# Performance work log

Hardware: AMD Instinct MI355X
Metric: run time of the kernel (lower is better)

## Reference

```python
import jax, jax.numpy as jnp
import numpy as np

B, S, D, H = 4, 2048, 1024, 16
DH = D // H  # 64


def setup_inputs() -> dict:
    key = jax.random.key(0)
    ks = jax.random.split(key, 7)
    scale = 1.0 / np.sqrt(DH)
    return {
        "sequences": jax.random.normal(ks[0], (B, S, D), dtype=jnp.float32),
        # torch Linear weights: [out, in] per head -> stacked [H, DH, DH]
        "Wq": jax.random.uniform(ks[1], (H, DH, DH), jnp.float32, -scale, scale),
        "bq": jax.random.uniform(ks[2], (H, DH), jnp.float32, -scale, scale),
        "Wk": jax.random.uniform(ks[3], (H, DH, DH), jnp.float32, -scale, scale),
        "bk": jax.random.uniform(ks[4], (H, DH), jnp.float32, -scale, scale),
        "Wv": jax.random.uniform(ks[5], (H, DH, DH), jnp.float32, -scale, scale),
        "bv": jax.random.uniform(ks[6], (H, DH), jnp.float32, -scale, scale),
    }


def reference(sequences, Wq, bq, Wk, bk, Wv, bv):
    # split d into heads: [B, S, H, DH]
    x = sequences.reshape(B, S, H, DH)
    # per-head Linear: y = x @ W.T + b
    q = jnp.einsum("bshd,hed->bshe", x, Wq) + bq
    k = jnp.einsum("bshd,hed->bshe", x, Wk) + bk
    v = jnp.einsum("bshd,hed->bshe", x, Wv) + bv
    # scaled dot-product attention per head
    scores = jnp.einsum("bshd,bthd->bhst", q, k) / jnp.sqrt(jnp.float32(DH))
    attn = jax.nn.softmax(scores, axis=-1)
    out = jnp.einsum("bhst,bthd->bshd", attn, v)
    # hstack heads back to [B, S, D]
    return out.reshape(B, S, D)
```

## Files before the change

kernel.cpp:

```cpp
#include <hip/hip_runtime.h>
#include <hip/hip_bf16.h>


typedef unsigned short u16;
typedef unsigned int   u32;
typedef float  f32x4  __attribute__((ext_vector_type(4)));
typedef __bf16 bf16x4 __attribute__((ext_vector_type(4)));
typedef __bf16 bf16x8 __attribute__((ext_vector_type(8)));

#define NB 4
#define SS 2048
#define DDIM 1024
#define NH 16
#define DH 64

static __device__ __forceinline__ float fexp2(float x) {
#if __has_builtin(__builtin_amdgcn_exp2f)
    return __builtin_amdgcn_exp2f(x);
#else
    return exp2f(x);
#endif
}
static __device__ __forceinline__ bf16x4 cvt4(f32x4 v) {
    return __builtin_convertvector(v, bf16x4);
}
static __device__ __forceinline__ bf16x8 cvt8(f32x4 lo, f32x4 hi) {
    return __builtin_shufflevector(cvt4(lo), cvt4(hi), 0, 1, 2, 3, 4, 5, 6, 7);
}

#define WST 72

__global__ __launch_bounds__(256) void qkv_kernel(
        const float* __restrict__ x,
        const float* __restrict__ Wq, const float* __restrict__ bq,
        const float* __restrict__ Wk, const float* __restrict__ bk,
        const float* __restrict__ Wv, const float* __restrict__ bv,
        u16* __restrict__ Qw, u16* __restrict__ Kw, u16* __restrict__ Vt) {
    __shared__ __align__(16) u16 W_lds[3 * DH * WST];

    const int tid  = threadIdx.x;
    const int w    = tid >> 6;
    const int lane = tid & 63;
    const int quad = lane >> 4;
    const int c    = lane & 15;
    const int bid  = blockIdx.x;
    const int bh   = bid & 63;
    const int s0   = (bid >> 6) * 256;
    const int b    = bh >> 4, h = bh & 15;

    {
        const float* Wsrc[3] = {Wq + h*DH*DH, Wk + h*DH*DH, Wv + h*DH*DH};
        #pragma unroll
        for (int j = 0; j < 6; ++j) {
            const int m = j >> 1;
            const int chunk = ((j & 1) << 8) + tid;
            const float* src = Wsrc[m] + chunk * 8;
            f32x4 lo = *(const f32x4*)src;
            f32x4 hi = *(const f32x4*)(src + 4);
            const int row = chunk >> 3, c8 = chunk & 7;
            *(bf16x8*)&W_lds[(m*DH + row) * WST + c8*8] = cvt8(lo, hi);
        }
    }
    __syncthreads();

    bf16x8 wf[3][4][2];
    #pragma unroll
    for (int m = 0; m < 3; ++m)
        #pragma unroll
        for (int mt = 0; mt < 4; ++mt)
            #pragma unroll
            for (int kh = 0; kh < 2; ++kh)
                wf[m][mt][kh] = *(const bf16x8*)&W_lds[(m*DH + mt*16 + c) * WST + kh*32 + quad*8];

    f32x4 biasQK[2][4];
    float biasV[4];
    #pragma unroll
    for (int mt = 0; mt < 4; ++mt) {
        biasQK[0][mt] = *(const f32x4*)(bq + h*DH + mt*16 + quad*4);
        biasQK[1][mt] = *(const f32x4*)(bk + h*DH + mt*16 + quad*4);
        biasV[mt] = bv[h*DH + mt*16 + c];
    }

    const size_t qkbase = (size_t)bh * SS * DH;
    const size_t vtbase = (size_t)bh * DH * SS;

    #pragma unroll 1
    for (int g = 0; g < 4; ++g) {
        const int sb = s0 + w*64 + g*16;
        const float* xr = x + ((size_t)(b * SS + sb + c)) * DDIM + h * DH;
        bf16x8 xb[2];
        #pragma unroll
        for (int kh = 0; kh < 2; ++kh) {
            f32x4 lo = *(const f32x4*)(xr + kh*32 + quad*8);
            f32x4 hi = *(const f32x4*)(xr + kh*32 + quad*8 + 4);
            xb[kh] = cvt8(lo, hi);
        }

        const int srow = sb + c;
        const int tq = srow & 31;
        const int sK = (srow & ~31) | ((tq & 4) << 2) | ((tq >> 3) << 2) | (tq & 3);

        #pragma unroll
        for (int m = 0; m < 2; ++m) {
            const float scale = (m == 0) ? 0.18033688f : 1.0f;
            u16* base = (m == 0 ? Qw : Kw) + qkbase + (size_t)(m == 0 ? srow : sK) * DH;
            #pragma unroll
            for (int mt = 0; mt < 4; ++mt) {
                f32x4 acc = {0.f, 0.f, 0.f, 0.f};
                acc = __builtin_amdgcn_mfma_f32_16x16x32_bf16(wf[m][mt][0], xb[0], acc, 0, 0, 0);
                acc = __builtin_amdgcn_mfma_f32_16x16x32_bf16(wf[m][mt][1], xb[1], acc, 0, 0, 0);
                f32x4 v = (acc + biasQK[m][mt]) * scale;
                *(bf16x4*)(base + mt*16 + quad*4) = cvt4(v);
            }
        }
        #pragma unroll
        for (int nt = 0; nt < 4; ++nt) {
            f32x4 acc = {0.f, 0.f, 0.f, 0.f};
            acc = __builtin_amdgcn_mfma_f32_16x16x32_bf16(xb[0], wf[2][nt][0], acc, 0, 0, 0);
            acc = __builtin_amdgcn_mfma_f32_16x16x32_bf16(xb[1], wf[2][nt][1], acc, 0, 0, 0);
            f32x4 v = acc + biasV[nt];
            u16* dst = Vt + vtbase + (size_t)(nt*16 + c) * SS + sb + quad*4;
            *(bf16x4*)dst = cvt4(v);
        }
    }
}

#define KT 128
#define KST 72
#define VST 136

#define LOAD_FRAGS(kf, vf, g) do {                                             \
        kf[0] = *(const bf16x8*)&Kl[((g)*32 + c) * KST + quad*8];              \
        kf[1] = *(const bf16x8*)&Kl[((g)*32 + c) * KST + 32 + quad*8];         \
        kf[2] = *(const bf16x8*)&Kl[((g)*32 + 16 + c) * KST + quad*8];         \
        kf[3] = *(const bf16x8*)&Kl[((g)*32 + 16 + c) * KST + 32 + quad*8];    \
        vf[0] = *(const bf16x8*)&Vl[( 0 + c) * VST + (g)*32 + quad*8];         \
        vf[1] = *(const bf16x8*)&Vl[(16 + c) * VST + (g)*32 + quad*8];         \
        vf[2] = *(const bf16x8*)&Vl[(32 + c) * VST + (g)*32 + quad*8];         \
        vf[3] = *(const bf16x8*)&Vl[(48 + c) * VST + (g)*32 + quad*8];         \
    } while (0)

#define COMPUTE_G(kf, vf) do {                                                 \
        __builtin_amdgcn_s_setprio(1);                                         \
        _Pragma("unroll")                                                      \
        for (int qt = 0; qt < 4; ++qt) {                                       \
            f32x4 sA = {0.f,0.f,0.f,0.f}, sB = {0.f,0.f,0.f,0.f};              \
            sA = __builtin_amdgcn_mfma_f32_16x16x32_bf16(kf[0], qf[qt][0], sA, 0,0,0); \
            sA = __builtin_amdgcn_mfma_f32_16x16x32_bf16(kf[1], qf[qt][1], sA, 0,0,0); \
            sB = __builtin_amdgcn_mfma_f32_16x16x32_bf16(kf[2], qf[qt][0], sB, 0,0,0); \
            sB = __builtin_amdgcn_mfma_f32_16x16x32_bf16(kf[3], qf[qt][1], sB, 0,0,0); \
            f32x4 eA, eB;                                                      \
            _Pragma("unroll")                                                  \
            for (int r = 0; r < 4; ++r) { eA[r] = fexp2(sA[r]); eB[r] = fexp2(sB[r]); } \
            bf16x8 pf = cvt8(eA, eB);                                          \
            o[0][qt] = __builtin_amdgcn_mfma_f32_16x16x32_bf16(vf[0], pf, o[0][qt], 0,0,0); \
            o[1][qt] = __builtin_amdgcn_mfma_f32_16x16x32_bf16(vf[1], pf, o[1][qt], 0,0,0); \
            o[2][qt] = __builtin_amdgcn_mfma_f32_16x16x32_bf16(vf[2], pf, o[2][qt], 0,0,0); \
            o[3][qt] = __builtin_amdgcn_mfma_f32_16x16x32_bf16(vf[3], pf, o[3][qt], 0,0,0); \
            lacc[qt] = __builtin_amdgcn_mfma_f32_16x16x32_bf16(ones8, pf, lacc[qt], 0,0,0); \
        }                                                                      \
        __builtin_amdgcn_s_setprio(0);                                         \
    } while (0)

__global__ __launch_bounds__(256, 2) void attn_kernel(
        const u16* __restrict__ Qw, const u16* __restrict__ Kw,
        const u16* __restrict__ Vt, float* __restrict__ out) {
    __shared__ __align__(16) u16 K_lds[2][KT * KST];
    __shared__ __align__(16) u16 V_lds[2][DH * VST];

    const int tid  = threadIdx.x;
    const int w    = tid >> 6;
    const int lane = tid & 63;
    const int quad = lane >> 4;
    const int c    = lane & 15;
    const int bid  = blockIdx.x;
    const int bh   = bid & 63;
    const int q0   = (bid >> 6) * 256;
    const int qw   = q0 + w * 64;

    const u16* Qb = Qw + (size_t)bh * SS * DH;
    const u16* Kb = Kw + (size_t)bh * SS * DH;
    const u16* Vb = Vt + (size_t)bh * DH * SS;

    bf16x8 qf[4][2];
    #pragma unroll
    for (int qt = 0; qt < 4; ++qt) {
        const u16* qrow = Qb + (size_t)(qw + qt*16 + c) * DH;
        qf[qt][0] = *(const bf16x8*)(qrow + quad*8);
        qf[qt][1] = *(const bf16x8*)(qrow + 32 + quad*8);
    }

    f32x4 o[4][4];
    f32x4 lacc[4];
    #pragma unroll
    for (int qt = 0; qt < 4; ++qt) {
        lacc[qt] = (f32x4){0.f, 0.f, 0.f, 0.f};
        #pragma unroll
        for (int dt = 0; dt < 4; ++dt) o[dt][qt] = (f32x4){0.f, 0.f, 0.f, 0.f};
    }

    bf16x8 ones8;
    { union { u16 u[8]; bf16x8 v; } one;
      #pragma unroll
      for (int i = 0; i < 8; ++i) one.u[i] = 0x3F80;
      ones8 = one.v; }

    const int krow = tid >> 1;
    const int kcol = (tid & 1) * 32;
    const int kofs = krow * KST + kcol;
    const int vrow = tid >> 2;
    const int vcol = (tid & 3) * 32;
    const int vofs = vrow * VST + vcol;

    uint4 kr0 = *(const uint4*)(Kb + (size_t)krow * DH + kcol);
    uint4 kr1 = *(const uint4*)(Kb + (size_t)krow * DH + kcol + 8);
    uint4 kr2 = *(const uint4*)(Kb + (size_t)krow * DH + kcol + 16);
    uint4 kr3 = *(const uint4*)(Kb + (size_t)krow * DH + kcol + 24);
    uint4 vr0 = *(const uint4*)(Vb + (size_t)vrow * SS + vcol);
    uint4 vr1 = *(const uint4*)(Vb + (size_t)vrow * SS + vcol + 8);
    uint4 vr2 = *(const uint4*)(Vb + (size_t)vrow * SS + vcol + 16);
    uint4 vr3 = *(const uint4*)(Vb + (size_t)vrow * SS + vcol + 24);

    #pragma unroll 1
    for (int t0 = 0; t0 < SS; t0 += KT) {
        const int bsel = (t0 >> 7) & 1;
        u16* Kl = K_lds[bsel];
        u16* Vl = V_lds[bsel];
        *(uint4*)&Kl[kofs]      = kr0;
        *(uint4*)&Kl[kofs + 8]  = kr1;
        *(uint4*)&Kl[kofs + 16] = kr2;
        *(uint4*)&Kl[kofs + 24] = kr3;
        *(uint4*)&Vl[vofs]      = vr0;
        *(uint4*)&Vl[vofs + 8]  = vr1;
        *(uint4*)&Vl[vofs + 16] = vr2;
        *(uint4*)&Vl[vofs + 24] = vr3;
        __syncthreads();
        int tn = t0 + KT; if (tn >= SS) tn = 0;
        kr0 = *(const uint4*)(Kb + (size_t)(tn + krow) * DH + kcol);
        kr1 = *(const uint4*)(Kb + (size_t)(tn + krow) * DH + kcol + 8);
        kr2 = *(const uint4*)(Kb + (size_t)(tn + krow) * DH + kcol + 16);
        kr3 = *(const uint4*)(Kb + (size_t)(tn + krow) * DH + kcol + 24);
        vr0 = *(const uint4*)(Vb + (size_t)vrow * SS + tn + vcol);
        vr1 = *(const uint4*)(Vb + (size_t)vrow * SS + tn + vcol + 8);
        vr2 = *(const uint4*)(Vb + (size_t)vrow * SS + tn + vcol + 16);
        vr3 = *(const uint4*)(Vb + (size_t)vrow * SS + tn + vcol + 24);

        bf16x8 kfA[4], vfA[4], kfB[4], vfB[4];
        LOAD_FRAGS(kfA, vfA, 0);
        LOAD_FRAGS(kfB, vfB, 1);
        COMPUTE_G(kfA, vfA);
        LOAD_FRAGS(kfA, vfA, 2);
        COMPUTE_G(kfB, vfB);
        LOAD_FRAGS(kfB, vfB, 3);
        COMPUTE_G(kfA, vfA);
        COMPUTE_G(kfB, vfB);
    }

    const int b = bh >> 4, h = bh & 15;
    #pragma unroll
    for (int qt = 0; qt < 4; ++qt) {
        const float inv = 1.0f / lacc[qt][0];
        const int token = qw + qt*16 + c;
        float* orow = out + ((size_t)b * SS + token) * DDIM + h * DH;
        #pragma unroll
        for (int dt = 0; dt < 4; ++dt) {
            f32x4 vv = o[dt][qt] * inv;
            *(f32x4*)(orow + dt*16 + quad*4) = vv;
        }
    }
}

extern "C" void kernel_launch(void* const* d_in, const int* in_sizes, int n_in,
                              void* d_out, int out_size, void* d_ws, size_t ws_size,
                              hipStream_t stream) {
    const float* x  = (const float*)d_in[0];
    const float* Wq = (const float*)d_in[1];
    const float* bq = (const float*)d_in[2];
    const float* Wk = (const float*)d_in[3];
    const float* bk = (const float*)d_in[4];
    const float* Wv = (const float*)d_in[5];
    const float* bv = (const float*)d_in[6];

    u16* Qw = (u16*)d_ws;
    u16* Kw = Qw + (size_t)NB * NH * SS * DH;
    u16* Vt = Kw + (size_t)NB * NH * SS * DH;

    qkv_kernel<<<64 * (SS / 256), 256, 0, stream>>>(
        x, Wq, bq, Wk, bk, Wv, bv, Qw, Kw, Vt);
    attn_kernel<<<64 * (SS / 256), 256, 0, stream>>>(Qw, Kw, Vt, (float*)d_out);
}
```

Measured before the change: 179.1 us.

## Switch attention inner loop to 32x32x16 MFMA tiles with VALU row sums

Replaces the 16x16x32 bf16 MFMA tiling in the attention kernel with 32x32x16 MFMAs for both QK^T and PV. The K-row permutation written by the projection kernel is changed so the score accumulator layout matches the PV operand layout. The softmax denominator is now summed with VALU adds plus a cross-half shuffle instead of an extra MFMA against a ones vector. The aim is fewer MFMA instructions and less fragment traffic per tile. The trade-off is larger 16-wide accumulators, which raise register pressure and may affect the two-blocks-per-CU occupancy target.

```diff
diff --git a/kernel.cpp b/kernel.cpp
--- a/kernel.cpp
+++ b/kernel.cpp
@@ -4,9 +4,10 @@
 
 typedef unsigned short u16;
 typedef unsigned int   u32;
-typedef float  f32x4  __attribute__((ext_vector_type(4)));
-typedef __bf16 bf16x4 __attribute__((ext_vector_type(4)));
-typedef __bf16 bf16x8 __attribute__((ext_vector_type(8)));
+typedef float  f32x4   __attribute__((ext_vector_type(4)));
+typedef float  f32x16  __attribute__((ext_vector_type(16)));
+typedef __bf16 bf16x4  __attribute__((ext_vector_type(4)));
+typedef __bf16 bf16x8  __attribute__((ext_vector_type(8)));
 
 #define NB 4
 #define SS 2048
@@ -98,7 +99,10 @@
 
         const int srow = sb + c;
         const int tq = srow & 31;
-        const int sK = (srow & ~31) | ((tq & 4) << 2) | ((tq >> 3) << 2) | (tq & 3);
+        const int sK = (srow & ~31) | (tq & 3)
+                     | (((tq >> 3) & 1) << 2)
+                     | (((tq >> 2) & 1) << 3)
+                     | (((tq >> 4) & 1) << 4);
 
         #pragma unroll
         for (int m = 0; m < 2; ++m) {
@@ -129,36 +133,41 @@
 #define KST 72
 #define VST 136
 
-#define LOAD_FRAGS(kf, vf, g) do {                                             \
-        kf[0] = *(const bf16x8*)&Kl[((g)*32 + c) * KST + quad*8];              \
-        kf[1] = *(const bf16x8*)&Kl[((g)*32 + c) * KST + 32 + quad*8];         \
-        kf[2] = *(const bf16x8*)&Kl[((g)*32 + 16 + c) * KST + quad*8];         \
-        kf[3] = *(const bf16x8*)&Kl[((g)*32 + 16 + c) * KST + 32 + quad*8];    \
-        vf[0] = *(const bf16x8*)&Vl[( 0 + c) * VST + (g)*32 + quad*8];         \
-        vf[1] = *(const bf16x8*)&Vl[(16 + c) * VST + (g)*32 + quad*8];         \
-        vf[2] = *(const bf16x8*)&Vl[(32 + c) * VST + (g)*32 + quad*8];         \
-        vf[3] = *(const bf16x8*)&Vl[(48 + c) * VST + (g)*32 + quad*8];         \
+#define Z16 {0.f,0.f,0.f,0.f,0.f,0.f,0.f,0.f,0.f,0.f,0.f,0.f,0.f,0.f,0.f,0.f}
+
+#define QT_BODY(qt, lp) do {                                                   \
+        f32x16 s = Z16;                                                        \
+        s = __builtin_amdgcn_mfma_f32_32x32x16_bf16(ka0, qf[qt][0], s, 0,0,0); \
+        s = __builtin_amdgcn_mfma_f32_32x32x16_bf16(ka1, qf[qt][1], s, 0,0,0); \
+        s = __builtin_amdgcn_mfma_f32_32x32x16_bf16(ka2, qf[qt][2], s, 0,0,0); \
+        s = __builtin_amdgcn_mfma_f32_32x32x16_bf16(ka3, qf[qt][3], s, 0,0,0); \
+        f32x16 e;                                                              \
+        _Pragma("unroll")                                                      \
+        for (int r = 0; r < 16; ++r) e[r] = fexp2(s[r]);                       \
+        lp += (((e[0]+e[1])+(e[2]+e[3])) + ((e[4]+e[5])+(e[6]+e[7])))          \
+            + (((e[8]+e[9])+(e[10]+e[11])) + ((e[12]+e[13])+(e[14]+e[15])));   \
+        bf16x8 pf0 = cvt8((f32x4){e[0],e[1],e[2],e[3]},                        \
+                          (f32x4){e[4],e[5],e[6],e[7]});                       \
+        bf16x8 pf1 = cvt8((f32x4){e[8],e[9],e[10],e[11]},                      \
+                          (f32x4){e[12],e[13],e[14],e[15]});                   \
+        o[0][qt] = __builtin_amdgcn_mfma_f32_32x32x16_bf16(vf00, pf0, o[0][qt], 0,0,0); \
+        o[0][qt] = __builtin_amdgcn_mfma_f32_32x32x16_bf16(vf01, pf1, o[0][qt], 0,0,0); \
+        o[1][qt] = __builtin_amdgcn_mfma_f32_32x32x16_bf16(vf10, pf0, o[1][qt], 0,0,0); \
+        o[1][qt] = __builtin_amdgcn_mfma_f32_32x32x16_bf16(vf11, pf1, o[1][qt], 0,0,0); \
     } while (0)
 
-#define COMPUTE_G(kf, vf) do {                                                 \
+#define GROUP(g) do {                                                          \
+        bf16x8 ka0 = *(const bf16x8*)&Kl[((g)*32 + l31) * KST +  0 + hi*8];    \
+        bf16x8 ka1 = *(const bf16x8*)&Kl[((g)*32 + l31) * KST + 16 + hi*8];    \
+        bf16x8 ka2 = *(const bf16x8*)&Kl[((g)*32 + l31) * KST + 32 + hi*8];    \
+        bf16x8 ka3 = *(const bf16x8*)&Kl[((g)*32 + l31) * KST + 48 + hi*8];    \
+        bf16x8 vf00 = *(const bf16x8*)&Vl[( 0 + l31) * VST + (g)*32 +  0 + hi*8]; \
+        bf16x8 vf01 = *(const bf16x8*)&Vl[( 0 + l31) * VST + (g)*32 + 16 + hi*8]; \
+        bf16x8 vf10 = *(const bf16x8*)&Vl[(32 + l31) * VST + (g)*32 +  0 + hi*8]; \
+        bf16x8 vf11 = *(const bf16x8*)&Vl[(32 + l31) * VST + (g)*32 + 16 + hi*8]; \
         __builtin_amdgcn_s_setprio(1);                                         \
-        _Pragma("unroll")                                                      \
-        for (int qt = 0; qt < 4; ++qt) {                                       \
-            f32x4 sA = {0.f,0.f,0.f,0.f}, sB = {0.f,0.f,0.f,0.f};              \
-            sA = __builtin_amdgcn_mfma_f32_16x16x32_bf16(kf[0], qf[qt][0], sA, 0,0,0); \
-            sA = __builtin_amdgcn_mfma_f32_16x16x32_bf16(kf[1], qf[qt][1], sA, 0,0,0); \
-            sB = __builtin_amdgcn_mfma_f32_16x16x32_bf16(kf[2], qf[qt][0], sB, 0,0,0); \
-            sB = __builtin_amdgcn_mfma_f32_16x16x32_bf16(kf[3], qf[qt][1], sB, 0,0,0); \
-            f32x4 eA, eB;                                                      \
-            _Pragma("unroll")                                                  \
-            for (int r = 0; r < 4; ++r) { eA[r] = fexp2(sA[r]); eB[r] = fexp2(sB[r]); } \
-            bf16x8 pf = cvt8(eA, eB);                                          \
-            o[0][qt] = __builtin_amdgcn_mfma_f32_16x16x32_bf16(vf[0], pf, o[0][qt], 0,0,0); \
-            o[1][qt] = __builtin_amdgcn_mfma_f32_16x16x32_bf16(vf[1], pf, o[1][qt], 0,0,0); \
-            o[2][qt] = __builtin_amdgcn_mfma_f32_16x16x32_bf16(vf[2], pf, o[2][qt], 0,0,0); \
-            o[3][qt] = __builtin_amdgcn_mfma_f32_16x16x32_bf16(vf[3], pf, o[3][qt], 0,0,0); \
-            lacc[qt] = __builtin_amdgcn_mfma_f32_16x16x32_bf16(ones8, pf, lacc[qt], 0,0,0); \
-        }                                                                      \
+        QT_BODY(0, lp0);                                                       \
+        QT_BODY(1, lp1);                                                       \
         __builtin_amdgcn_s_setprio(0);                                         \
     } while (0)
 
@@ -171,8 +180,8 @@
     const int tid  = threadIdx.x;
     const int w    = tid >> 6;
     const int lane = tid & 63;
-    const int quad = lane >> 4;
-    const int c    = lane & 15;
+    const int l31  = lane & 31;
+    const int hi   = lane >> 5;
     const int bid  = blockIdx.x;
     const int bh   = bid & 63;
     const int q0   = (bid >> 6) * 256;
@@ -182,28 +191,21 @@
     const u16* Kb = Kw + (size_t)bh * SS * DH;
     const u16* Vb = Vt + (size_t)bh * DH * SS;
 
-    bf16x8 qf[4][2];
-    #pragma unroll
-    for (int qt = 0; qt < 4; ++qt) {
-        const u16* qrow = Qb + (size_t)(qw + qt*16 + c) * DH;
-        qf[qt][0] = *(const bf16x8*)(qrow + quad*8);
-        qf[qt][1] = *(const bf16x8*)(qrow + 32 + quad*8);
-    }
-
-    f32x4 o[4][4];
-    f32x4 lacc[4];
-    #pragma unroll
-    for (int qt = 0; qt < 4; ++qt) {
-        lacc[qt] = (f32x4){0.f, 0.f, 0.f, 0.f};
-        #pragma unroll
-        for (int dt = 0; dt < 4; ++dt) o[dt][qt] = (f32x4){0.f, 0.f, 0.f, 0.f};
-    }
-
-    bf16x8 ones8;
-    { union { u16 u[8]; bf16x8 v; } one;
-      #pragma unroll
-      for (int i = 0; i < 8; ++i) one.u[i] = 0x3F80;
-      ones8 = one.v; }
+    bf16x8 qf[2][4];
+    #pragma unroll
+    for (int qt = 0; qt < 2; ++qt) {
+        const u16* qrow = Qb + (size_t)(qw + qt*32 + l31) * DH;
+        #pragma unroll
+        for (int m = 0; m < 4; ++m)
+            qf[qt][m] = *(const bf16x8*)(qrow + m*16 + hi*8);
+    }
+
+    f32x16 o[2][2];
+    #pragma unroll
+    for (int dt = 0; dt < 2; ++dt)
+        #pragma unroll
+        for (int qt = 0; qt < 2; ++qt) o[dt][qt] = (f32x16)Z16;
+    float lp0 = 0.f, lp1 = 0.f;
 
     const int krow = tid >> 1;
     const int kcol = (tid & 1) * 32;
@@ -245,27 +247,29 @@
         vr2 = *(const uint4*)(Vb + (size_t)vrow * SS + tn + vcol + 16);
         vr3 = *(const uint4*)(Vb + (size_t)vrow * SS + tn + vcol + 24);
 
-        bf16x8 kfA[4], vfA[4], kfB[4], vfB[4];
-        LOAD_FRAGS(kfA, vfA, 0);
-        LOAD_FRAGS(kfB, vfB, 1);
-        COMPUTE_G(kfA, vfA);
-        LOAD_FRAGS(kfA, vfA, 2);
-        COMPUTE_G(kfB, vfB);
-        LOAD_FRAGS(kfB, vfB, 3);
-        COMPUTE_G(kfA, vfA);
-        COMPUTE_G(kfB, vfB);
+        GROUP(0);
+        GROUP(1);
+        GROUP(2);
+        GROUP(3);
     }
 
     const int b = bh >> 4, h = bh & 15;
-    #pragma unroll
-    for (int qt = 0; qt < 4; ++qt) {
-        const float inv = 1.0f / lacc[qt][0];
-        const int token = qw + qt*16 + c;
+    const float lw0 = lp0 + __shfl_xor(lp0, 32, 64);
+    const float lw1 = lp1 + __shfl_xor(lp1, 32, 64);
+    #pragma unroll
+    for (int qt = 0; qt < 2; ++qt) {
+        const float inv = 1.0f / (qt == 0 ? lw0 : lw1);
+        const int token = qw + qt*32 + l31;
         float* orow = out + ((size_t)b * SS + token) * DDIM + h * DH;
         #pragma unroll
-        for (int dt = 0; dt < 4; ++dt) {
-            f32x4 vv = o[dt][qt] * inv;
-            *(f32x4*)(orow + dt*16 + quad*4) = vv;
+        for (int dt = 0; dt < 2; ++dt) {
+            #pragma unroll
+            for (int rq = 0; rq < 4; ++rq) {
+                f32x4 vv = {o[dt][qt][4*rq+0], o[dt][qt][4*rq+1],
+                            o[dt][qt][4*rq+2], o[dt][qt][4*rq+3]};
+                vv = vv * inv;
+                *(f32x4*)(orow + dt*32 + 8*rq + 4*hi) = vv;
+            }
         }
     }
 }
```

After: 255.8 us. 1.43x slower.

## Halve QKV block rows, issue x loads before barrier, stream weights from LDS

Applied to the files above, without the earlier changes.

The QKV projection kernel now gives each block 128 rows instead of 256, so twice as many blocks launch. Each wave handles two 16-row groups at once with no loop. All x loads are issued before the barrier so they overlap the weight staging into LDS. Weight fragments are read from LDS at each use rather than held in registers, which lowers register pressure but adds LDS reads, and each block now repeats the per-block weight conversion for half as many rows.

```diff
diff --git a/kernel.cpp b/kernel.cpp
--- a/kernel.cpp
+++ b/kernel.cpp
@@ -45,7 +45,7 @@
     const int c    = lane & 15;
     const int bid  = blockIdx.x;
     const int bh   = bid & 63;
-    const int s0   = (bid >> 6) * 256;
+    const int s0   = (bid >> 6) * 128;
     const int b    = bh >> 4, h = bh & 15;
 
     {
@@ -61,16 +61,19 @@
             *(bf16x8*)&W_lds[(m*DH + row) * WST + c8*8] = cvt8(lo, hi);
         }
     }
-    __syncthreads();
-
-    bf16x8 wf[3][4][2];
-    #pragma unroll
-    for (int m = 0; m < 3; ++m)
-        #pragma unroll
-        for (int mt = 0; mt < 4; ++mt)
-            #pragma unroll
-            for (int kh = 0; kh < 2; ++kh)
-                wf[m][mt][kh] = *(const bf16x8*)&W_lds[(m*DH + mt*16 + c) * WST + kh*32 + quad*8];
+
+    const int sbA = s0 + w*32;
+    const int sbB = sbA + 16;
+    const float* xrA = x + ((size_t)(b * SS + sbA + c)) * DDIM + h * DH;
+    const float* xrB = x + ((size_t)(b * SS + sbB + c)) * DDIM + h * DH;
+    f32x4 a0 = *(const f32x4*)(xrA + quad*8);
+    f32x4 a1 = *(const f32x4*)(xrA + quad*8 + 4);
+    f32x4 a2 = *(const f32x4*)(xrA + 32 + quad*8);
+    f32x4 a3 = *(const f32x4*)(xrA + 32 + quad*8 + 4);
+    f32x4 b0 = *(const f32x4*)(xrB + quad*8);
+    f32x4 b1 = *(const f32x4*)(xrB + quad*8 + 4);
+    f32x4 b2 = *(const f32x4*)(xrB + 32 + quad*8);
+    f32x4 b3 = *(const f32x4*)(xrB + 32 + quad*8 + 4);
 
     f32x4 biasQK[2][4];
     float biasV[4];
@@ -81,47 +84,56 @@
         biasV[mt] = bv[h*DH + mt*16 + c];
     }
 
+    __syncthreads();
+
+    bf16x8 xbA[2] = { cvt8(a0, a1), cvt8(a2, a3) };
+    bf16x8 xbB[2] = { cvt8(b0, b1), cvt8(b2, b3) };
+
     const size_t qkbase = (size_t)bh * SS * DH;
     const size_t vtbase = (size_t)bh * DH * SS;
 
-    #pragma unroll 1
-    for (int g = 0; g < 4; ++g) {
-        const int sb = s0 + w*64 + g*16;
-        const float* xr = x + ((size_t)(b * SS + sb + c)) * DDIM + h * DH;
-        bf16x8 xb[2];
+    const int srowA = sbA + c, srowB = sbB + c;
+    const int tqA = srowA & 31, tqB = srowB & 31;
+    const int sKA = (srowA & ~31) | ((tqA & 4) << 2) | ((tqA >> 3) << 2) | (tqA & 3);
+    const int sKB = (srowB & ~31) | ((tqB & 4) << 2) | ((tqB >> 3) << 2) | (tqB & 3);
+
+    #pragma unroll
+    for (int m = 0; m < 2; ++m) {
+        const float scale = (m == 0) ? 0.18033688f : 1.0f;
+        u16* baseA = (m == 0 ? Qw : Kw) + qkbase + (size_t)(m == 0 ? srowA : sKA) * DH;
+        u16* baseB = (m == 0 ? Qw : Kw) + qkbase + (size_t)(m == 0 ? srowB : sKB) * DH;
         #pragma unroll
-        for (int kh = 0; kh < 2; ++kh) {
-            f32x4 lo = *(const f32x4*)(xr + kh*32 + quad*8);
-            f32x4 hi = *(const f32x4*)(xr + kh*32 + quad*8 + 4);
-            xb[kh] = cvt8(lo, hi);
+        for (int mt = 0; mt < 4; ++mt) {
+            const bf16x8 w0 = *(const bf16x8*)&W_lds[(m*DH + mt*16 + c) * WST + quad*8];
+            const bf16x8 w1 = *(const bf16x8*)&W_lds[(m*DH + mt*16 + c) * WST + 32 + quad*8];
+            f32x4 accA = {0.f, 0.f, 0.f, 0.f};
+            accA = __builtin_amdgcn_mfma_f32_16x16x32_bf16(w0, xbA[0], accA, 0, 0, 0);
+            accA = __builtin_amdgcn_mfma_f32_16x16x32_bf16(w1, xbA[1], accA, 0, 0, 0);
+            f32x4 accB = {0.f, 0.f, 0.f, 0.f};
+            accB = __builtin_amdgcn_mfma_f32_16x16x32_bf16(w0, xbB[0], accB, 0, 0, 0);
+            accB = __builtin_amdgcn_mfma_f32_16x16x32_bf16(w1, xbB[1], accB, 0, 0, 0);
+            f32x4 vA = (accA + biasQK[m][mt]) * scale;
+            f32x4 vB = (accB + biasQK[m][mt]) * scale;
+            *(bf16x4*)(baseA + mt*16 + quad*4) = cvt4(vA);
+            *(bf16x4*)(baseB + mt*16 + quad*4) = cvt4(vB);
         }
-
-        const int srow = sb + c;
-        const int tq = srow & 31;
-        const int sK = (srow & ~31) | ((tq & 4) << 2) | ((tq >> 3) << 2) | (tq & 3);
-
-        #pragma unroll
-        for (int m = 0; m < 2; ++m) {
-            const float scale = (m == 0) ? 0.18033688f : 1.0f;
-            u16* base = (m == 0 ? Qw : Kw) + qkbase + (size_t)(m == 0 ? srow : sK) * DH;
-            #pragma unroll
-            for (int mt = 0; mt < 4; ++mt) {
-                f32x4 acc = {0.f, 0.f, 0.f, 0.f};
-                acc = __builtin_amdgcn_mfma_f32_16x16x32_bf16(wf[m][mt][0], xb[0], acc, 0, 0, 0);
-                acc = __builtin_amdgcn_mfma_f32_16x16x32_bf16(wf[m][mt][1], xb[1], acc, 0, 0, 0);
-                f32x4 v = (acc + biasQK[m][mt]) * scale;
-                *(bf16x4*)(base + mt*16 + quad*4) = cvt4(v);
-            }
-        }
-        #pragma unroll
-        for (int nt = 0; nt < 4; ++nt) {
-            f32x4 acc = {0.f, 0.f, 0.f, 0.f};
-            acc = __builtin_amdgcn_mfma_f32_16x16x32_bf16(xb[0], wf[2][nt][0], acc, 0, 0, 0);
-            acc = __builtin_amdgcn_mfma_f32_16x16x32_bf16(xb[1], wf[2][nt][1], acc, 0, 0, 0);
-            f32x4 v = acc + biasV[nt];
-            u16* dst = Vt + vtbase + (size_t)(nt*16 + c) * SS + sb + quad*4;
-            *(bf16x4*)dst = cvt4(v);
-        }
+    }
+    #pragma unroll
+    for (int nt = 0; nt < 4; ++nt) {
+        const bf16x8 w0 = *(const bf16x8*)&W_lds[(2*DH + nt*16 + c) * WST + quad*8];
+        const bf16x8 w1 = *(const bf16x8*)&W_lds[(2*DH + nt*16 + c) * WST + 32 + quad*8];
+        f32x4 accA = {0.f, 0.f, 0.f, 0.f};
+        accA = __builtin_amdgcn_mfma_f32_16x16x32_bf16(xbA[0], w0, accA, 0, 0, 0);
+        accA = __builtin_amdgcn_mfma_f32_16x16x32_bf16(xbA[1], w1, accA, 0, 0, 0);
+        f32x4 accB = {0.f, 0.f, 0.f, 0.f};
+        accB = __builtin_amdgcn_mfma_f32_16x16x32_bf16(xbB[0], w0, accB, 0, 0, 0);
+        accB = __builtin_amdgcn_mfma_f32_16x16x32_bf16(xbB[1], w1, accB, 0, 0, 0);
+        f32x4 vA = accA + biasV[nt];
+        f32x4 vB = accB + biasV[nt];
+        u16* dstA = Vt + vtbase + (size_t)(nt*16 + c) * SS + sbA + quad*4;
+        u16* dstB = Vt + vtbase + (size_t)(nt*16 + c) * SS + sbB + quad*4;
+        *(bf16x4*)dstA = cvt4(vA);
+        *(bf16x4*)dstB = cvt4(vB);
     }
 }
 
@@ -285,7 +297,7 @@
     u16* Kw = Qw + (size_t)NB * NH * SS * DH;
     u16* Vt = Kw + (size_t)NB * NH * SS * DH;
 
-    qkv_kernel<<<64 * (SS / 256), 256, 0, stream>>>(
+    qkv_kernel<<<64 * (SS / 128), 256, 0, stream>>>(
         x, Wq, bq, Wk, bk, Wv, bv, Qw, Kw, Vt);
     attn_kernel<<<64 * (SS / 256), 256, 0, stream>>>(Qw, Kw, Vt, (float*)d_out);
 }
```

New measurement: 169.7 us. -5.3%, faster.
